# Kernel optimization log

Hardware: AMD Instinct MI355X
Metric: run time of the kernel (lower is better)

## Reference

```python
import jax, jax.numpy as jnp
import numpy as np

N_COARSE, N_FINE, N_EDGE, W, DEPTH = 16384, 65536, 393216, 128, 2


def _mlp_params(key, fan_in, width, out):
    k1, k2 = jax.random.split(key)
    w1 = jax.random.normal(k1, (fan_in, width), jnp.float32) / np.sqrt(fan_in)
    b1 = jnp.zeros((width,), jnp.float32)
    w2 = jax.random.normal(k2, (width, out), jnp.float32) / np.sqrt(width)
    b2 = jnp.zeros((out,), jnp.float32)
    return w1, b1, w2, b2


def setup_inputs() -> dict:
    key = jax.random.key(0)
    ks = jax.random.split(key, 16)
    v = jax.random.normal(ks[0], (N_COARSE, W), jnp.float32)
    c_skip = jax.random.normal(ks[1], (N_FINE, W), jnp.float32)
    e_skip = jax.random.normal(ks[2], (N_EDGE, W), jnp.float32)
    edge_index_skip = jax.random.randint(ks[3], (2, N_EDGE), 0, N_FINE, jnp.int32)
    batch_skip = jnp.zeros((N_FINE,), jnp.int32)  # single graph
    cluster = jax.random.randint(ks[4], (N_FINE,), 0, N_COARSE, jnp.int32)
    rel_pos = jax.random.normal(ks[5], (N_FINE, 1), jnp.float32)  # scalar rel pos (scalar_rel_pos=True)

    # unpooling FNN: (W + 1) -> W -> W
    uw1, ub1, uw2, ub2 = _mlp_params(ks[6], W + 1, W, W)
    # InteractionNetwork MLPs, stacked over DEPTH layers
    ew1 = []; eb1 = []; ew2 = []; eb2 = []
    nw1 = []; nb1 = []; nw2 = []; nb2 = []
    for i in range(DEPTH):
        a, b, c, d = _mlp_params(ks[7 + i], 3 * W, W, W)  # edge MLP: [e, v_s, v_r]
        ew1.append(a); eb1.append(b); ew2.append(c); eb2.append(d)
        a, b, c, d = _mlp_params(ks[9 + i], 2 * W, W, W)  # node MLP: [v, aggr(e)]
        nw1.append(a); nb1.append(b); nw2.append(c); nb2.append(d)
    stk = lambda xs: jnp.stack(xs, 0)
    return {
        'v': v, 'c_skip': c_skip, 'e_skip': e_skip, 'rel_pos': rel_pos,
        'unpool_w1': uw1, 'unpool_b1': ub1, 'unpool_w2': uw2, 'unpool_b2': ub2,
        'edge_w1': stk(ew1), 'edge_b1': stk(eb1), 'edge_w2': stk(ew2), 'edge_b2': stk(eb2),
        'node_w1': stk(nw1), 'node_b1': stk(nb1), 'node_w2': stk(nw2), 'node_b2': stk(nb2),
        'edge_index_skip': edge_index_skip, 'cluster': cluster, 'batch_skip': batch_skip,
    }


def _mlp(x, w1, b1, w2, b2):
    return jax.nn.selu(x @ w1 + b1) @ w2 + b2


def reference(v, c_skip, e_skip, rel_pos,
              unpool_w1, unpool_b1, unpool_w2, unpool_b2,
              edge_w1, edge_b1, edge_w2, edge_b2,
              node_w1, node_b1, node_w2, node_b2,
              edge_index_skip, cluster, batch_skip):
    # --- MeshUpMP: gather coarse features to fine nodes, mix with rel. pos. ---
    h = jnp.concatenate([v[cluster], rel_pos], axis=-1)            # [N_fine, W+1]
    v = _mlp(h, unpool_w1, unpool_b1, unpool_w2, unpool_b2)        # [N_fine, W]
    v = v + c_skip
    e = e_skip
    s, r = edge_index_skip[0], edge_index_skip[1]
    n_nodes = v.shape[0]
    # --- stacked InteractionNetwork layers (residual edge+node updates) ---
    for i in range(edge_w1.shape[0]):
        msg = jnp.concatenate([e, v[s], v[r]], axis=-1)            # [E, 3W]
        e = e + _mlp(msg, edge_w1[i], edge_b1[i], edge_w2[i], edge_b2[i])
        agg = jax.ops.segment_sum(e, r, num_segments=n_nodes)      # sum aggregation
        nin = jnp.concatenate([v, agg], axis=-1)                   # [N, 2W]
        v = v + _mlp(nin, node_w1[i], node_b1[i], node_w2[i], node_b2[i])
    return v
```

## Files before the change

kernel.cpp:

```cpp
#include <hip/hip_runtime.h>
#include <hip/hip_bf16.h>
#include <stdint.h>

#define NCOARSE 16384
#define NFINE   65536
#define NEDGE   393216

typedef __bf16 bf16;
typedef bf16 bf16x8 __attribute__((ext_vector_type(8)));
typedef bf16 bf16x4 __attribute__((ext_vector_type(4)));
typedef float f32x4 __attribute__((ext_vector_type(4)));

__device__ __forceinline__ float selu_f(float x) {
    return x > 0.f ? 1.0507009873554805f * x
                   : 1.7580993408473766f * (__expf(x) - 1.f);
}

__device__ __forceinline__ bf16x8 cvt8(f32x4 lo, f32x4 hi) {
    bf16x8 r;
    r[0] = (bf16)lo[0]; r[1] = (bf16)lo[1]; r[2] = (bf16)lo[2]; r[3] = (bf16)lo[3];
    r[4] = (bf16)hi[0]; r[5] = (bf16)hi[1]; r[6] = (bf16)hi[2]; r[7] = (bf16)hi[3];
    return r;
}

__global__ void prep_weights(const float* __restrict__ uw1, const float* __restrict__ uw2,
                             const float* __restrict__ ew1, const float* __restrict__ ew2,
                             const float* __restrict__ nw1, const float* __restrict__ nw2,
                             bf16* __restrict__ wb)
{
    int i = blockIdx.x * 256 + threadIdx.x;
    float v;
    if (i < 16384) {
        int j = i; int k = (j >> 12) * 32 + (j & 31), n = (j & 4095) >> 5;
        v = uw1[k * 128 + n];
    } else if (i < 32768) {
        int j = i - 16384; int k = (j >> 12) * 32 + (j & 31), n = (j & 4095) >> 5;
        v = uw2[k * 128 + n];
    } else if (i < 131072) {
        int j = i - 32768; int l = j / 49152; j -= l * 49152;
        int k = (j >> 12) * 32 + (j & 31), n = (j & 4095) >> 5;
        v = ew1[l * 49152 + k * 128 + n];
    } else if (i < 163840) {
        int j = i - 131072; int l = j >> 14; j &= 16383;
        int k = (j >> 12) * 32 + (j & 31), n = (j & 4095) >> 5;
        v = ew2[l * 16384 + k * 128 + n];
    } else if (i < 229376) {
        int j = i - 163840; int l = j >> 15; j &= 32767;
        int k = (j >> 12) * 32 + (j & 31), n = (j & 4095) >> 5;
        v = nw1[l * 32768 + k * 128 + n];
    } else {
        int j = i - 229376; int l = j >> 14; j &= 16383;
        int k = (j >> 12) * 32 + (j & 31), n = (j & 4095) >> 5;
        v = nw2[l * 16384 + k * 128 + n];
    }
    wb[i] = (bf16)v;
}

__global__ void hist_kernel(const int* __restrict__ ei, int* __restrict__ cnt) {
    int e = blockIdx.x * 256 + threadIdx.x;
    if (e < NEDGE) atomicAdd(&cnt[ei[NEDGE + e]], 1);
}

__global__ __launch_bounds__(1024)
void scan_kernel(const int* __restrict__ cnt, int* __restrict__ rowptr,
                 int* __restrict__ cursor) {
    __shared__ int part[1024];
    const int t = threadIdx.x;
    const int base = t * 64;
    int s = 0;
    for (int i = 0; i < 64; ++i) s += cnt[base + i];
    part[t] = s;
    __syncthreads();
    for (int off = 1; off < 1024; off <<= 1) {
        int v = (t >= off) ? part[t - off] : 0;
        __syncthreads();
        part[t] += v;
        __syncthreads();
    }
    int run = part[t] - s;
    for (int i = 0; i < 64; ++i) {
        int c = cnt[base + i];
        rowptr[base + i] = run;
        cursor[base + i] = run;
        run += c;
    }
    if (t == 1023) rowptr[65536] = run;
}

__global__ void scatter_kernel(const int* __restrict__ ei, int* __restrict__ cursor,
                               int* __restrict__ perm) {
    int e = blockIdx.x * 256 + threadIdx.x;
    if (e < NEDGE) {
        int r = ei[NEDGE + e];
        int p = atomicAdd(&cursor[r], 1);
        perm[p] = e;
    }
}

__global__ __launch_bounds__(256)
void agg_kernel(const bf16* __restrict__ e, const int* __restrict__ rowptr,
                const int* __restrict__ perm, bf16* __restrict__ agg) {
    int t = blockIdx.x * 256 + threadIdx.x;
    int node = t >> 3, c0 = (t & 7) * 16;
    int s = rowptr[node], en = rowptr[node + 1];
    float acc[16];
    #pragma unroll
    for (int k = 0; k < 16; ++k) acc[k] = 0.f;
    for (int j = s; j < en; ++j) {
        size_t ed = (size_t)perm[j];
        bf16x8 x0 = *(const bf16x8*)(e + ed * 128 + c0);
        bf16x8 x1 = *(const bf16x8*)(e + ed * 128 + c0 + 8);
        #pragma unroll
        for (int k = 0; k < 8; ++k) { acc[k] += (float)x0[k]; acc[8 + k] += (float)x1[k]; }
    }
    bf16x8 o0, o1;
    #pragma unroll
    for (int k = 0; k < 8; ++k) { o0[k] = (bf16)acc[k]; o1[k] = (bf16)acc[8 + k]; }
    *(bf16x8*)(agg + (size_t)node * 128 + c0) = o0;
    *(bf16x8*)(agg + (size_t)node * 128 + c0 + 8) = o1;
}


#define STAGE_LOAD(wp, st0, st1) do { \
    st0 = *(const bf16x8*)((wp) + tid * 8); \
    st1 = *(const bf16x8*)((wp) + 2048 + tid * 8); } while (0)
#define STAGE_WRITE(buf, st0, st1) do { \
    *(bf16x8*)&(buf)[tid >> 2][(tid & 3) * 8] = st0; \
    *(bf16x8*)&(buf)[(tid + 256) >> 2][(tid & 3) * 8] = st1; } while (0)

template<bool EF32>
__global__ __launch_bounds__(256, 2)
void edge_kernel(const void* __restrict__ e_in_v,
                 bf16* __restrict__ e_out,
                 const bf16* __restrict__ v_bf,
                 const int* __restrict__ ei,
                 const bf16* __restrict__ w1s,
                 const float* __restrict__ b1,
                 const bf16* __restrict__ w2s,
                 const float* __restrict__ b2)
{
    const int tid = threadIdx.x;
    const int wv = tid >> 6, lane = tid & 63;
    const int lr = lane & 15, g = lane >> 4;
    const int wbase = blockIdx.x * 128 + wv * 32;

    __shared__ bf16 wl[2][128][40];
    __shared__ bf16 hid_all[4][32][136];
    bf16 (*hid)[136] = hid_all[wv];

    const float* e_f32 = (const float*)e_in_v;
    const bf16*  e_b16 = (const bf16*)e_in_v;

    int row[2], sidx[2], ridx[2];
    #pragma unroll
    for (int mt = 0; mt < 2; ++mt) {
        row[mt] = wbase + mt * 16 + lr;
        sidx[mt] = ei[row[mt]];
        ridx[mt] = ei[NEDGE + row[mt]];
    }

    bf16x8 be[4][2], bs[4][2], br[4][2];
    #pragma unroll
    for (int ks = 0; ks < 4; ++ks)
        #pragma unroll
        for (int mt = 0; mt < 2; ++mt)
            bs[ks][mt] = *(const bf16x8*)(v_bf + (size_t)sidx[mt] * 128 + ks * 32 + g * 8);
    #pragma unroll
    for (int ks = 0; ks < 4; ++ks)
        #pragma unroll
        for (int mt = 0; mt < 2; ++mt)
            br[ks][mt] = *(const bf16x8*)(v_bf + (size_t)ridx[mt] * 128 + ks * 32 + g * 8);
    if (EF32) {
        f32x4 tlo[4][2], thi[4][2];
        #pragma unroll
        for (int ks = 0; ks < 4; ++ks)
            #pragma unroll
            for (int mt = 0; mt < 2; ++mt) {
                const float* p = e_f32 + (size_t)row[mt] * 128 + ks * 32 + g * 8;
                tlo[ks][mt] = *(const f32x4*)p;
                thi[ks][mt] = *(const f32x4*)(p + 4);
            }
        #pragma unroll
        for (int ks = 0; ks < 4; ++ks)
            #pragma unroll
            for (int mt = 0; mt < 2; ++mt)
                be[ks][mt] = cvt8(tlo[ks][mt], thi[ks][mt]);
    } else {
        #pragma unroll
        for (int ks = 0; ks < 4; ++ks)
            #pragma unroll
            for (int mt = 0; mt < 2; ++mt)
                be[ks][mt] = *(const bf16x8*)(e_b16 + (size_t)row[mt] * 128 + ks * 32 + g * 8);
    }

    bf16x8 st0, st1;
    STAGE_LOAD(w1s, st0, st1);
    STAGE_WRITE(wl[0], st0, st1);
    __syncthreads();

    f32x4 acc1[8][2], acc2[8][2];
    #pragma unroll
    for (int oc = 0; oc < 8; ++oc) {
        f32x4 z = {0.f, 0.f, 0.f, 0.f};
        acc1[oc][0] = z; acc1[oc][1] = z;
    }

    f32x4  eof[8][2];
    bf16x4 eob[8][2];

    #pragma unroll
    for (int s = 0; s < 16; ++s) {
        const int cur = s & 1;
        if (s < 15) {
            const bf16* wp = (s + 1 < 12) ? w1s + (size_t)(s + 1) * 4096
                                          : w2s + (size_t)(s + 1 - 12) * 4096;
            STAGE_LOAD(wp, st0, st1);
        }
        if (s == 12) {
            #pragma unroll
            for (int mt = 0; mt < 2; ++mt)
                #pragma unroll
                for (int oc = 0; oc < 8; ++oc) {
                    const int col = oc * 16 + g * 4;
                    if (EF32) eof[oc][mt] = *(const f32x4*)(e_f32 + (size_t)row[mt] * 128 + col);
                    else      eob[oc][mt] = *(const bf16x4*)(e_b16 + (size_t)row[mt] * 128 + col);
                }
        }
        bf16x8 a[8];
        #pragma unroll
        for (int oc = 0; oc < 8; ++oc)
            a[oc] = *(const bf16x8*)&wl[cur][oc * 16 + lr][g * 8];

        if (s < 12) {
            bf16x8 b0 = (s < 4) ? be[s][0] : (s < 8) ? bs[s - 4][0] : br[s - 8][0];
            bf16x8 b1f = (s < 4) ? be[s][1] : (s < 8) ? bs[s - 4][1] : br[s - 8][1];
            #pragma unroll
            for (int oc = 0; oc < 8; ++oc) {
                acc1[oc][0] = __builtin_amdgcn_mfma_f32_16x16x32_bf16(a[oc], b0, acc1[oc][0], 0, 0, 0);
                acc1[oc][1] = __builtin_amdgcn_mfma_f32_16x16x32_bf16(a[oc], b1f, acc1[oc][1], 0, 0, 0);
            }
        } else {
            if (s == 12) {
                #pragma unroll
                for (int oc = 0; oc < 8; ++oc) {
                    f32x4 z = {0.f, 0.f, 0.f, 0.f};
                    acc2[oc][0] = z; acc2[oc][1] = z;
                }
            }
            bf16x8 h0 = *(const bf16x8*)&hid[lr][(s - 12) * 32 + g * 8];
            bf16x8 h1 = *(const bf16x8*)&hid[16 + lr][(s - 12) * 32 + g * 8];
            #pragma unroll
            for (int oc = 0; oc < 8; ++oc) {
                acc2[oc][0] = __builtin_amdgcn_mfma_f32_16x16x32_bf16(a[oc], h0, acc2[oc][0], 0, 0, 0);
                acc2[oc][1] = __builtin_amdgcn_mfma_f32_16x16x32_bf16(a[oc], h1, acc2[oc][1], 0, 0, 0);
            }
        }
        if (s == 11) {
            #pragma unroll
            for (int mt = 0; mt < 2; ++mt)
                #pragma unroll
                for (int oc = 0; oc < 8; ++oc) {
                    const int col = oc * 16 + g * 4;
                    f32x4 bv = *(const f32x4*)(b1 + col);
                    bf16x4 h;
                    #pragma unroll
                    for (int j = 0; j < 4; ++j)
                        h[j] = (bf16)selu_f(acc1[oc][mt][j] + bv[j]);
                    *(bf16x4*)&hid[mt * 16 + lr][col] = h;
                }
        }
        if (s < 15) STAGE_WRITE(wl[cur ^ 1], st0, st1);
        __syncthreads();
    }

    #pragma unroll
    for (int mt = 0; mt < 2; ++mt) {
        const size_t r = row[mt];
        #pragma unroll
        for (int oc = 0; oc < 8; ++oc) {
            const int col = oc * 16 + g * 4;
            f32x4 b2v = *(const f32x4*)(b2 + col);
            bf16x4 stv;
            #pragma unroll
            for (int j = 0; j < 4; ++j) {
                float eo = EF32 ? eof[oc][mt][j] : (float)eob[oc][mt][j];
                stv[j] = (bf16)(eo + acc2[oc][mt][j] + b2v[j]);
            }
            __builtin_nontemporal_store(stv, (bf16x4*)(e_out + r * 128 + col));
        }
    }
}

__global__ __launch_bounds__(256, 2)
void node_kernel(float* __restrict__ v_io,
                 bf16* __restrict__ v_bf,
                 const bf16* __restrict__ agg,
                 const bf16* __restrict__ w1s,
                 const float* __restrict__ b1,
                 const bf16* __restrict__ w2s,
                 const float* __restrict__ b2)
{
    const int tid = threadIdx.x;
    const int wv = tid >> 6, lane = tid & 63;
    const int lr = lane & 15, g = lane >> 4;
    const int wbase = blockIdx.x * 128 + wv * 32;

    __shared__ bf16 wl[2][128][40];
    __shared__ bf16 hid_all[4][32][136];
    bf16 (*hid)[136] = hid_all[wv];

    int row[2];
    row[0] = wbase + lr; row[1] = wbase + 16 + lr;

    bf16x8 bv[4][2], ba[4][2];
    #pragma unroll
    for (int ks = 0; ks < 4; ++ks)
        #pragma unroll
        for (int mt = 0; mt < 2; ++mt)
            bv[ks][mt] = *(const bf16x8*)(v_bf + (size_t)row[mt] * 128 + ks * 32 + g * 8);
    #pragma unroll
    for (int ks = 0; ks < 4; ++ks)
        #pragma unroll
        for (int mt = 0; mt < 2; ++mt)
            ba[ks][mt] = *(const bf16x8*)(agg + (size_t)row[mt] * 128 + ks * 32 + g * 8);

    bf16x8 st0, st1;
    STAGE_LOAD(w1s, st0, st1);
    STAGE_WRITE(wl[0], st0, st1);
    __syncthreads();

    f32x4 acc1[8][2], acc2[8][2], vo[8][2];
    #pragma unroll
    for (int oc = 0; oc < 8; ++oc) {
        f32x4 z = {0.f, 0.f, 0.f, 0.f};
        acc1[oc][0] = z; acc1[oc][1] = z;
    }

    #pragma unroll
    for (int s = 0; s < 12; ++s) {
        const int cur = s & 1;
        if (s < 11) {
            const bf16* wp = (s + 1 < 8) ? w1s + (size_t)(s + 1) * 4096
                                         : w2s + (size_t)(s + 1 - 8) * 4096;
            STAGE_LOAD(wp, st0, st1);
        }
        if (s == 8) {
            #pragma unroll
            for (int mt = 0; mt < 2; ++mt)
                #pragma unroll
                for (int oc = 0; oc < 8; ++oc)
                    vo[oc][mt] = *(const f32x4*)(v_io + (size_t)row[mt] * 128 + oc * 16 + g * 4);
        }
        bf16x8 a[8];
        #pragma unroll
        for (int oc = 0; oc < 8; ++oc)
            a[oc] = *(const bf16x8*)&wl[cur][oc * 16 + lr][g * 8];

        if (s < 8) {
            bf16x8 b0 = (s < 4) ? bv[s][0] : ba[s - 4][0];
            bf16x8 b1f = (s < 4) ? bv[s][1] : ba[s - 4][1];
            #pragma unroll
            for (int oc = 0; oc < 8; ++oc) {
                acc1[oc][0] = __builtin_amdgcn_mfma_f32_16x16x32_bf16(a[oc], b0, acc1[oc][0], 0, 0, 0);
                acc1[oc][1] = __builtin_amdgcn_mfma_f32_16x16x32_bf16(a[oc], b1f, acc1[oc][1], 0, 0, 0);
            }
        } else {
            if (s == 8) {
                #pragma unroll
                for (int oc = 0; oc < 8; ++oc) {
                    f32x4 z = {0.f, 0.f, 0.f, 0.f};
                    acc2[oc][0] = z; acc2[oc][1] = z;
                }
            }
            bf16x8 h0 = *(const bf16x8*)&hid[lr][(s - 8) * 32 + g * 8];
            bf16x8 h1 = *(const bf16x8*)&hid[16 + lr][(s - 8) * 32 + g * 8];
            #pragma unroll
            for (int oc = 0; oc < 8; ++oc) {
                acc2[oc][0] = __builtin_amdgcn_mfma_f32_16x16x32_bf16(a[oc], h0, acc2[oc][0], 0, 0, 0);
                acc2[oc][1] = __builtin_amdgcn_mfma_f32_16x16x32_bf16(a[oc], h1, acc2[oc][1], 0, 0, 0);
            }
        }
        if (s == 7) {
            #pragma unroll
            for (int mt = 0; mt < 2; ++mt)
                #pragma unroll
                for (int oc = 0; oc < 8; ++oc) {
                    const int col = oc * 16 + g * 4;
                    f32x4 bvv = *(const f32x4*)(b1 + col);
                    bf16x4 h;
                    #pragma unroll
                    for (int j = 0; j < 4; ++j)
                        h[j] = (bf16)selu_f(acc1[oc][mt][j] + bvv[j]);
                    *(bf16x4*)&hid[mt * 16 + lr][col] = h;
                }
        }
        if (s < 11) STAGE_WRITE(wl[cur ^ 1], st0, st1);
        __syncthreads();
    }

    #pragma unroll
    for (int mt = 0; mt < 2; ++mt) {
        const size_t r = row[mt];
        #pragma unroll
        for (int oc = 0; oc < 8; ++oc) {
            const int col = oc * 16 + g * 4;
            f32x4 b2v = *(const f32x4*)(b2 + col);
            f32x4 vn; bf16x4 m;
            #pragma unroll
            for (int j = 0; j < 4; ++j) {
                vn[j] = vo[oc][mt][j] + acc2[oc][mt][j] + b2v[j];
                m[j] = (bf16)vn[j];
            }
            *(f32x4*)(v_io + r * 128 + col) = vn;
            *(bf16x4*)(v_bf + r * 128 + col) = m;
        }
    }
}

__global__ __launch_bounds__(256, 2)
void unpool_kernel(const float* __restrict__ v_coarse,
                   const float* __restrict__ c_skip,
                   const float* __restrict__ rel_pos,
                   const float* __restrict__ uw1,
                   const float* __restrict__ b1,
                   const bf16* __restrict__ w1s,
                   const bf16* __restrict__ w2s,
                   const float* __restrict__ b2,
                   const int* __restrict__ cluster,
                   float* __restrict__ v_out,
                   bf16* __restrict__ v_bf)
{
    const int tid = threadIdx.x;
    const int wv = tid >> 6, lane = tid & 63;
    const int lr = lane & 15, g = lane >> 4;
    const int wbase = blockIdx.x * 128 + wv * 32;

    __shared__ bf16 wl[2][128][40];
    __shared__ bf16 hid_all[4][32][136];
    bf16 (*hid)[136] = hid_all[wv];

    int row[2], cl[2]; float relv[2];
    #pragma unroll
    for (int mt = 0; mt < 2; ++mt) {
        row[mt] = wbase + mt * 16 + lr;
        cl[mt] = cluster[row[mt]];
        relv[mt] = rel_pos[row[mt]];
    }

    bf16x8 bfr[4][2];
    {
        f32x4 tlo[4][2], thi[4][2];
        #pragma unroll
        for (int ks = 0; ks < 4; ++ks)
            #pragma unroll
            for (int mt = 0; mt < 2; ++mt) {
                const float* p = v_coarse + (size_t)cl[mt] * 128 + ks * 32 + g * 8;
                tlo[ks][mt] = *(const f32x4*)p;
                thi[ks][mt] = *(const f32x4*)(p + 4);
            }
        #pragma unroll
        for (int ks = 0; ks < 4; ++ks)
            #pragma unroll
            for (int mt = 0; mt < 2; ++mt)
                bfr[ks][mt] = cvt8(tlo[ks][mt], thi[ks][mt]);
    }

    bf16x8 st0, st1;
    STAGE_LOAD(w1s, st0, st1);
    STAGE_WRITE(wl[0], st0, st1);
    __syncthreads();

    f32x4 acc1[8][2], acc2[8][2], cs[8][2];
    #pragma unroll
    for (int oc = 0; oc < 8; ++oc) {
        f32x4 z = {0.f, 0.f, 0.f, 0.f};
        acc1[oc][0] = z; acc1[oc][1] = z;
    }

    #pragma unroll
    for (int s = 0; s < 8; ++s) {
        const int cur = s & 1;
        if (s < 7) {
            const bf16* wp = (s + 1 < 4) ? w1s + (size_t)(s + 1) * 4096
                                         : w2s + (size_t)(s + 1 - 4) * 4096;
            STAGE_LOAD(wp, st0, st1);
        }
        if (s == 4) {
            #pragma unroll
            for (int mt = 0; mt < 2; ++mt)
                #pragma unroll
                for (int oc = 0; oc < 8; ++oc)
                    cs[oc][mt] = *(const f32x4*)(c_skip + (size_t)row[mt] * 128 + oc * 16 + g * 4);
        }
        bf16x8 a[8];
        #pragma unroll
        for (int oc = 0; oc < 8; ++oc)
            a[oc] = *(const bf16x8*)&wl[cur][oc * 16 + lr][g * 8];

        if (s < 4) {
            #pragma unroll
            for (int oc = 0; oc < 8; ++oc) {
                acc1[oc][0] = __builtin_amdgcn_mfma_f32_16x16x32_bf16(a[oc], bfr[s][0], acc1[oc][0], 0, 0, 0);
                acc1[oc][1] = __builtin_amdgcn_mfma_f32_16x16x32_bf16(a[oc], bfr[s][1], acc1[oc][1], 0, 0, 0);
            }
        } else {
            if (s == 4) {
                #pragma unroll
                for (int oc = 0; oc < 8; ++oc) {
                    f32x4 z = {0.f, 0.f, 0.f, 0.f};
                    acc2[oc][0] = z; acc2[oc][1] = z;
                }
            }
            bf16x8 h0 = *(const bf16x8*)&hid[lr][(s - 4) * 32 + g * 8];
            bf16x8 h1 = *(const bf16x8*)&hid[16 + lr][(s - 4) * 32 + g * 8];
            #pragma unroll
            for (int oc = 0; oc < 8; ++oc) {
                acc2[oc][0] = __builtin_amdgcn_mfma_f32_16x16x32_bf16(a[oc], h0, acc2[oc][0], 0, 0, 0);
                acc2[oc][1] = __builtin_amdgcn_mfma_f32_16x16x32_bf16(a[oc], h1, acc2[oc][1], 0, 0, 0);
            }
        }
        if (s == 3) {
            #pragma unroll
            for (int mt = 0; mt < 2; ++mt)
                #pragma unroll
                for (int oc = 0; oc < 8; ++oc) {
                    const int col = oc * 16 + g * 4;
                    f32x4 bvv = *(const f32x4*)(b1 + col);
                    f32x4 wlr = *(const f32x4*)(uw1 + 128 * 128 + col);
                    bf16x4 h;
                    #pragma unroll
                    for (int j = 0; j < 4; ++j)
                        h[j] = (bf16)selu_f(acc1[oc][mt][j] + bvv[j] + relv[mt] * wlr[j]);
                    *(bf16x4*)&hid[mt * 16 + lr][col] = h;
                }
        }
        if (s < 7) STAGE_WRITE(wl[cur ^ 1], st0, st1);
        __syncthreads();
    }

    #pragma unroll
    for (int mt = 0; mt < 2; ++mt) {
        const size_t r = row[mt];
        #pragma unroll
        for (int oc = 0; oc < 8; ++oc) {
            const int col = oc * 16 + g * 4;
            f32x4 b2v = *(const f32x4*)(b2 + col);
            f32x4 vn; bf16x4 m;
            #pragma unroll
            for (int j = 0; j < 4; ++j) {
                vn[j] = acc2[oc][mt][j] + b2v[j] + cs[oc][mt][j];
                m[j] = (bf16)vn[j];
            }
            *(f32x4*)(v_out + r * 128 + col) = vn;
            *(bf16x4*)(v_bf + r * 128 + col) = m;
        }
    }
}

extern "C" void kernel_launch(void* const* d_in, const int* in_sizes, int n_in,
                              void* d_out, int out_size, void* d_ws, size_t ws_size,
                              hipStream_t stream) {
    const float* v_c    = (const float*)d_in[0];
    const float* c_skip = (const float*)d_in[1];
    const float* e_skip = (const float*)d_in[2];
    const float* rel    = (const float*)d_in[3];
    const float* uw1    = (const float*)d_in[4];
    const float* ub1    = (const float*)d_in[5];
    const float* uw2    = (const float*)d_in[6];
    const float* ub2    = (const float*)d_in[7];
    const float* ew1    = (const float*)d_in[8];
    const float* eb1    = (const float*)d_in[9];
    const float* ew2    = (const float*)d_in[10];
    const float* eb2    = (const float*)d_in[11];
    const float* nw1    = (const float*)d_in[12];
    const float* nb1    = (const float*)d_in[13];
    const float* nw2    = (const float*)d_in[14];
    const float* nb2    = (const float*)d_in[15];
    const int*   ei     = (const int*)d_in[16];
    const int*   clus   = (const int*)d_in[17];

    char* ws = (char*)d_ws;
    bf16*  e_bf   = (bf16*)(ws);
    bf16*  v_bf   = (bf16*)(ws + 100663296);
    bf16*  agg    = (bf16*)(ws + 117440512);
    bf16*  wb     = (bf16*)(ws + 134217728);
    int*   cnt    = (int*) (ws + 134742016);
    int*   rowptr = (int*) (ws + 135004160);
    int*   cursor = (int*) (ws + 135266308);
    int*   perm   = (int*) (ws + 135528452);

    float* vout = (float*)d_out;

    prep_weights<<<1024, 256, 0, stream>>>(uw1, uw2, ew1, ew2, nw1, nw2, wb);
    hipMemsetAsync(cnt, 0, 262144, stream);
    hist_kernel<<<1536, 256, 0, stream>>>(ei, cnt);
    scan_kernel<<<1, 1024, 0, stream>>>(cnt, rowptr, cursor);
    scatter_kernel<<<1536, 256, 0, stream>>>(ei, cursor, perm);

    unpool_kernel<<<512, 256, 0, stream>>>(v_c, c_skip, rel, uw1, ub1,
                                           wb + 0, wb + 16384, ub2, clus, vout, v_bf);

    edge_kernel<true><<<3072, 256, 0, stream>>>((const void*)e_skip, e_bf, v_bf, ei,
                                                wb + 32768, eb1, wb + 131072, eb2);
    agg_kernel<<<2048, 256, 0, stream>>>(e_bf, rowptr, perm, agg);
    node_kernel<<<512, 256, 0, stream>>>(vout, v_bf, agg,
                                         wb + 163840, nb1, wb + 229376, nb2);

    edge_kernel<false><<<3072, 256, 0, stream>>>((const void*)e_bf, e_bf, v_bf, ei,
                                                 wb + 32768 + 49152, eb1 + 128,
                                                 wb + 131072 + 16384, eb2 + 128);
    agg_kernel<<<2048, 256, 0, stream>>>(e_bf, rowptr, perm, agg);
    node_kernel<<<512, 256, 0, stream>>>(vout, v_bf, agg,
                                         wb + 163840 + 32768, nb1 + 128, wb + 229376 + 16384, nb2 + 128);
}
```

Before: 553.4 us.

## Make edge kernel persistent with LDS-resident W1 and register-resident W2

The edge MLP kernel becomes persistent: 256 blocks each load the whole first-layer weight matrix once into LDS, in a new k-inner layout produced by prep_weights. Each lane keeps its second-layer weight fragments in registers. Each wave then loops over 12 edge tiles, prefetching the next tile's edge features and gathered node rows while computing the current one. This removes the per-tile weight staging and per-step block barriers of the old double-buffered pipeline. The cost is one 4-wave block per CU, which leaves little occupancy to hide gather latency, plus heavy register pressure. The output store also changes from nontemporal to a plain store.

```diff
diff --git a/kernel.cpp b/kernel.cpp
--- a/kernel.cpp
+++ b/kernel.cpp
@@ -38,7 +38,8 @@
         v = uw2[k * 128 + n];
     } else if (i < 131072) {
         int j = i - 32768; int l = j / 49152; j -= l * 49152;
-        int k = (j >> 12) * 32 + (j & 31), n = (j & 4095) >> 5;
+        int seg = j >> 12, g = (j >> 10) & 3, n = (j >> 3) & 127, kk = j & 7;
+        int k = seg * 32 + g * 8 + kk;
         v = ew1[l * 49152 + k * 128 + n];
     } else if (i < 163840) {
         int j = i - 131072; int l = j >> 14; j &= 16383;
@@ -120,21 +121,22 @@
     *(bf16x8*)(agg + (size_t)node * 128 + c0 + 8) = o1;
 }
 
-
-#define STAGE_LOAD(wp, st0, st1) do { \
-    st0 = *(const bf16x8*)((wp) + tid * 8); \
-    st1 = *(const bf16x8*)((wp) + 2048 + tid * 8); } while (0)
-#define STAGE_WRITE(buf, st0, st1) do { \
-    *(bf16x8*)&(buf)[tid >> 2][(tid & 3) * 8] = st0; \
-    *(bf16x8*)&(buf)[(tid + 256) >> 2][(tid & 3) * 8] = st1; } while (0)
+__device__ __forceinline__ void load_v2(bf16x8 (&dst)[4][2], const bf16* __restrict__ v,
+                                        const int idx0, const int idx1, int g) {
+    #pragma unroll
+    for (int ks = 0; ks < 4; ++ks) {
+        dst[ks][0] = *(const bf16x8*)(v + (size_t)idx0 * 128 + ks * 32 + g * 8);
+        dst[ks][1] = *(const bf16x8*)(v + (size_t)idx1 * 128 + ks * 32 + g * 8);
+    }
+}
 
 template<bool EF32>
-__global__ __launch_bounds__(256, 2)
+__global__ __launch_bounds__(256, 1)
 void edge_kernel(const void* __restrict__ e_in_v,
                  bf16* __restrict__ e_out,
                  const bf16* __restrict__ v_bf,
                  const int* __restrict__ ei,
-                 const bf16* __restrict__ w1s,
+                 const bf16* __restrict__ w1g,
                  const float* __restrict__ b1,
                  const bf16* __restrict__ w2s,
                  const float* __restrict__ b2)
@@ -142,154 +144,189 @@
     const int tid = threadIdx.x;
     const int wv = tid >> 6, lane = tid & 63;
     const int lr = lane & 15, g = lane >> 4;
-    const int wbase = blockIdx.x * 128 + wv * 32;
-
-    __shared__ bf16 wl[2][128][40];
+
+    __shared__ bf16 wl[49152];
     __shared__ bf16 hid_all[4][32][136];
     bf16 (*hid)[136] = hid_all[wv];
 
     const float* e_f32 = (const float*)e_in_v;
     const bf16*  e_b16 = (const bf16*)e_in_v;
 
-    int row[2], sidx[2], ridx[2];
-    #pragma unroll
-    for (int mt = 0; mt < 2; ++mt) {
-        row[mt] = wbase + mt * 16 + lr;
-        sidx[mt] = ei[row[mt]];
-        ridx[mt] = ei[NEDGE + row[mt]];
-    }
-
-    bf16x8 be[4][2], bs[4][2], br[4][2];
-    #pragma unroll
-    for (int ks = 0; ks < 4; ++ks)
+    #pragma unroll
+    for (int c = 0; c < 24; ++c)
+        *(bf16x8*)&wl[c * 2048 + tid * 8] = *(const bf16x8*)(w1g + c * 2048 + tid * 8);
+
+    bf16x8 a2[4][8];
+    #pragma unroll
+    for (int s2 = 0; s2 < 4; ++s2)
+        #pragma unroll
+        for (int oc = 0; oc < 8; ++oc)
+            a2[s2][oc] = *(const bf16x8*)(w2s + s2 * 4096 + (oc * 16 + lr) * 32 + g * 8);
+
+    __syncthreads();
+
+    int tile = blockIdx.x * 48 + wv;
+
+    int rowC0, rowC1;
+    bf16x8 beC[4][2], bsC[4][2], brC[4][2];
+
+    {
+        rowC0 = tile * 32 + lr;
+        rowC1 = tile * 32 + 16 + lr;
+        int s0 = ei[rowC0], s1 = ei[rowC1];
+        int r0 = ei[NEDGE + rowC0], r1 = ei[NEDGE + rowC1];
+        if (EF32) {
+            #pragma unroll
+            for (int ks = 0; ks < 4; ++ks) {
+                const float* p0 = e_f32 + (size_t)rowC0 * 128 + ks * 32 + g * 8;
+                const float* p1 = e_f32 + (size_t)rowC1 * 128 + ks * 32 + g * 8;
+                beC[ks][0] = cvt8(*(const f32x4*)p0, *(const f32x4*)(p0 + 4));
+                beC[ks][1] = cvt8(*(const f32x4*)p1, *(const f32x4*)(p1 + 4));
+            }
+        } else {
+            #pragma unroll
+            for (int ks = 0; ks < 4; ++ks) {
+                beC[ks][0] = *(const bf16x8*)(e_b16 + (size_t)rowC0 * 128 + ks * 32 + g * 8);
+                beC[ks][1] = *(const bf16x8*)(e_b16 + (size_t)rowC1 * 128 + ks * 32 + g * 8);
+            }
+        }
+        load_v2(bsC, v_bf, s0, s1, g);
+        load_v2(brC, v_bf, r0, r1, g);
+    }
+
+    #pragma clang loop unroll(disable)
+    for (int i = 0; i < 12; ++i) {
+        const int ntile = tile + 4;
+        const bool more = (i < 11);
+
+        int rowN0 = 0, rowN1 = 0, sN0 = 0, sN1 = 0, rN0 = 0, rN1 = 0;
+        if (more) {
+            rowN0 = ntile * 32 + lr;
+            rowN1 = ntile * 32 + 16 + lr;
+            sN0 = ei[rowN0]; sN1 = ei[rowN1];
+            rN0 = ei[NEDGE + rowN0]; rN1 = ei[NEDGE + rowN1];
+        }
+
+        f32x4 acc1[8][2];
+        #pragma unroll
+        for (int oc = 0; oc < 8; ++oc) {
+            f32x4 z = {0.f, 0.f, 0.f, 0.f};
+            acc1[oc][0] = z; acc1[oc][1] = z;
+        }
+        #pragma unroll
+        for (int seg = 0; seg < 12; ++seg) {
+            bf16x8 b0 = (seg < 4) ? beC[seg & 3][0] : (seg < 8) ? bsC[seg & 3][0] : brC[seg & 3][0];
+            bf16x8 b1f = (seg < 4) ? beC[seg & 3][1] : (seg < 8) ? bsC[seg & 3][1] : brC[seg & 3][1];
+            #pragma unroll
+            for (int oc = 0; oc < 8; ++oc) {
+                bf16x8 a = *(const bf16x8*)&wl[(seg * 4 + g) * 1024 + (oc * 16 + lr) * 8];
+                acc1[oc][0] = __builtin_amdgcn_mfma_f32_16x16x32_bf16(a, b0, acc1[oc][0], 0, 0, 0);
+                acc1[oc][1] = __builtin_amdgcn_mfma_f32_16x16x32_bf16(a, b1f, acc1[oc][1], 0, 0, 0);
+            }
+        }
+
+        bf16x8 beN[4][2], bsN[4][2], brN[4][2];
+        if (more) {
+            if (EF32) {
+                #pragma unroll
+                for (int ks = 0; ks < 4; ++ks) {
+                    const float* p0 = e_f32 + (size_t)rowN0 * 128 + ks * 32 + g * 8;
+                    const float* p1 = e_f32 + (size_t)rowN1 * 128 + ks * 32 + g * 8;
+                    beN[ks][0] = cvt8(*(const f32x4*)p0, *(const f32x4*)(p0 + 4));
+                    beN[ks][1] = cvt8(*(const f32x4*)p1, *(const f32x4*)(p1 + 4));
+                }
+            } else {
+                #pragma unroll
+                for (int ks = 0; ks < 4; ++ks) {
+                    beN[ks][0] = *(const bf16x8*)(e_b16 + (size_t)rowN0 * 128 + ks * 32 + g * 8);
+                    beN[ks][1] = *(const bf16x8*)(e_b16 + (size_t)rowN1 * 128 + ks * 32 + g * 8);
+                }
+            }
+            load_v2(bsN, v_bf, sN0, sN1, g);
+            load_v2(brN, v_bf, rN0, rN1, g);
+        }
+
         #pragma unroll
         for (int mt = 0; mt < 2; ++mt)
-            bs[ks][mt] = *(const bf16x8*)(v_bf + (size_t)sidx[mt] * 128 + ks * 32 + g * 8);
-    #pragma unroll
-    for (int ks = 0; ks < 4; ++ks)
-        #pragma unroll
-        for (int mt = 0; mt < 2; ++mt)
-            br[ks][mt] = *(const bf16x8*)(v_bf + (size_t)ridx[mt] * 128 + ks * 32 + g * 8);
-    if (EF32) {
-        f32x4 tlo[4][2], thi[4][2];
-        #pragma unroll
-        for (int ks = 0; ks < 4; ++ks)
-            #pragma unroll
-            for (int mt = 0; mt < 2; ++mt) {
-                const float* p = e_f32 + (size_t)row[mt] * 128 + ks * 32 + g * 8;
-                tlo[ks][mt] = *(const f32x4*)p;
-                thi[ks][mt] = *(const f32x4*)(p + 4);
-            }
-        #pragma unroll
-        for (int ks = 0; ks < 4; ++ks)
-            #pragma unroll
-            for (int mt = 0; mt < 2; ++mt)
-                be[ks][mt] = cvt8(tlo[ks][mt], thi[ks][mt]);
-    } else {
-        #pragma unroll
-        for (int ks = 0; ks < 4; ++ks)
-            #pragma unroll
-            for (int mt = 0; mt < 2; ++mt)
-                be[ks][mt] = *(const bf16x8*)(e_b16 + (size_t)row[mt] * 128 + ks * 32 + g * 8);
-    }
-
-    bf16x8 st0, st1;
-    STAGE_LOAD(w1s, st0, st1);
-    STAGE_WRITE(wl[0], st0, st1);
-    __syncthreads();
-
-    f32x4 acc1[8][2], acc2[8][2];
-    #pragma unroll
-    for (int oc = 0; oc < 8; ++oc) {
-        f32x4 z = {0.f, 0.f, 0.f, 0.f};
-        acc1[oc][0] = z; acc1[oc][1] = z;
-    }
-
-    f32x4  eof[8][2];
-    bf16x4 eob[8][2];
-
-    #pragma unroll
-    for (int s = 0; s < 16; ++s) {
-        const int cur = s & 1;
-        if (s < 15) {
-            const bf16* wp = (s + 1 < 12) ? w1s + (size_t)(s + 1) * 4096
-                                          : w2s + (size_t)(s + 1 - 12) * 4096;
-            STAGE_LOAD(wp, st0, st1);
-        }
-        if (s == 12) {
-            #pragma unroll
-            for (int mt = 0; mt < 2; ++mt)
-                #pragma unroll
-                for (int oc = 0; oc < 8; ++oc) {
-                    const int col = oc * 16 + g * 4;
-                    if (EF32) eof[oc][mt] = *(const f32x4*)(e_f32 + (size_t)row[mt] * 128 + col);
-                    else      eob[oc][mt] = *(const bf16x4*)(e_b16 + (size_t)row[mt] * 128 + col);
-                }
-        }
-        bf16x8 a[8];
-        #pragma unroll
-        for (int oc = 0; oc < 8; ++oc)
-            a[oc] = *(const bf16x8*)&wl[cur][oc * 16 + lr][g * 8];
-
-        if (s < 12) {
-            bf16x8 b0 = (s < 4) ? be[s][0] : (s < 8) ? bs[s - 4][0] : br[s - 8][0];
-            bf16x8 b1f = (s < 4) ? be[s][1] : (s < 8) ? bs[s - 4][1] : br[s - 8][1];
-            #pragma unroll
-            for (int oc = 0; oc < 8; ++oc) {
-                acc1[oc][0] = __builtin_amdgcn_mfma_f32_16x16x32_bf16(a[oc], b0, acc1[oc][0], 0, 0, 0);
-                acc1[oc][1] = __builtin_amdgcn_mfma_f32_16x16x32_bf16(a[oc], b1f, acc1[oc][1], 0, 0, 0);
-            }
-        } else {
-            if (s == 12) {
-                #pragma unroll
-                for (int oc = 0; oc < 8; ++oc) {
-                    f32x4 z = {0.f, 0.f, 0.f, 0.f};
-                    acc2[oc][0] = z; acc2[oc][1] = z;
-                }
-            }
-            bf16x8 h0 = *(const bf16x8*)&hid[lr][(s - 12) * 32 + g * 8];
-            bf16x8 h1 = *(const bf16x8*)&hid[16 + lr][(s - 12) * 32 + g * 8];
-            #pragma unroll
-            for (int oc = 0; oc < 8; ++oc) {
-                acc2[oc][0] = __builtin_amdgcn_mfma_f32_16x16x32_bf16(a[oc], h0, acc2[oc][0], 0, 0, 0);
-                acc2[oc][1] = __builtin_amdgcn_mfma_f32_16x16x32_bf16(a[oc], h1, acc2[oc][1], 0, 0, 0);
-            }
-        }
-        if (s == 11) {
-            #pragma unroll
-            for (int mt = 0; mt < 2; ++mt)
-                #pragma unroll
-                for (int oc = 0; oc < 8; ++oc) {
-                    const int col = oc * 16 + g * 4;
-                    f32x4 bv = *(const f32x4*)(b1 + col);
-                    bf16x4 h;
-                    #pragma unroll
-                    for (int j = 0; j < 4; ++j)
-                        h[j] = (bf16)selu_f(acc1[oc][mt][j] + bv[j]);
-                    *(bf16x4*)&hid[mt * 16 + lr][col] = h;
-                }
-        }
-        if (s < 15) STAGE_WRITE(wl[cur ^ 1], st0, st1);
-        __syncthreads();
-    }
-
-    #pragma unroll
-    for (int mt = 0; mt < 2; ++mt) {
-        const size_t r = row[mt];
+            #pragma unroll
+            for (int oc = 0; oc < 8; ++oc) {
+                const int col = oc * 16 + g * 4;
+                f32x4 bv = *(const f32x4*)(b1 + col);
+                bf16x4 h;
+                #pragma unroll
+                for (int j = 0; j < 4; ++j)
+                    h[j] = (bf16)selu_f(acc1[oc][mt][j] + bv[j]);
+                *(bf16x4*)&hid[mt * 16 + lr][col] = h;
+            }
+
+        f32x4  eof[8][2];
+        bf16x4 eob[8][2];
+        #pragma unroll
+        for (int mt = 0; mt < 2; ++mt) {
+            const size_t r = (mt == 0) ? (size_t)rowC0 : (size_t)rowC1;
+            #pragma unroll
+            for (int oc = 0; oc < 8; ++oc) {
+                const int col = oc * 16 + g * 4;
+                if (EF32) eof[oc][mt] = *(const f32x4*)(e_f32 + r * 128 + col);
+                else      eob[oc][mt] = *(const bf16x4*)(e_b16 + r * 128 + col);
+            }
+        }
+
+        f32x4 acc2[8][2];
         #pragma unroll
         for (int oc = 0; oc < 8; ++oc) {
-            const int col = oc * 16 + g * 4;
-            f32x4 b2v = *(const f32x4*)(b2 + col);
-            bf16x4 stv;
-            #pragma unroll
-            for (int j = 0; j < 4; ++j) {
-                float eo = EF32 ? eof[oc][mt][j] : (float)eob[oc][mt][j];
-                stv[j] = (bf16)(eo + acc2[oc][mt][j] + b2v[j]);
-            }
-            __builtin_nontemporal_store(stv, (bf16x4*)(e_out + r * 128 + col));
-        }
-    }
-}
+            f32x4 z = {0.f, 0.f, 0.f, 0.f};
+            acc2[oc][0] = z; acc2[oc][1] = z;
+        }
+        #pragma unroll
+        for (int s2 = 0; s2 < 4; ++s2) {
+            bf16x8 h0 = *(const bf16x8*)&hid[lr][s2 * 32 + g * 8];
+            bf16x8 h1 = *(const bf16x8*)&hid[16 + lr][s2 * 32 + g * 8];
+            #pragma unroll
+            for (int oc = 0; oc < 8; ++oc) {
+                acc2[oc][0] = __builtin_amdgcn_mfma_f32_16x16x32_bf16(a2[s2][oc], h0, acc2[oc][0], 0, 0, 0);
+                acc2[oc][1] = __builtin_amdgcn_mfma_f32_16x16x32_bf16(a2[s2][oc], h1, acc2[oc][1], 0, 0, 0);
+            }
+        }
+
+        #pragma unroll
+        for (int mt = 0; mt < 2; ++mt) {
+            const size_t r = (mt == 0) ? (size_t)rowC0 : (size_t)rowC1;
+            #pragma unroll
+            for (int oc = 0; oc < 8; ++oc) {
+                const int col = oc * 16 + g * 4;
+                f32x4 b2v = *(const f32x4*)(b2 + col);
+                bf16x4 stv;
+                #pragma unroll
+                for (int j = 0; j < 4; ++j) {
+                    float eo = EF32 ? eof[oc][mt][j] : (float)eob[oc][mt][j];
+                    stv[j] = (bf16)(eo + acc2[oc][mt][j] + b2v[j]);
+                }
+                *(bf16x4*)(e_out + r * 128 + col) = stv;
+            }
+        }
+
+        if (more) {
+            #pragma unroll
+            for (int ks = 0; ks < 4; ++ks)
+                #pragma unroll
+                for (int mt = 0; mt < 2; ++mt) {
+                    beC[ks][mt] = beN[ks][mt];
+                    bsC[ks][mt] = bsN[ks][mt];
+                    brC[ks][mt] = brN[ks][mt];
+                }
+            rowC0 = rowN0; rowC1 = rowN1;
+        }
+        tile = ntile;
+    }
+}
+
+#define STAGE_LOAD(wp, st0, st1) do { \
+    st0 = *(const bf16x8*)((wp) + tid * 8); \
+    st1 = *(const bf16x8*)((wp) + 2048 + tid * 8); } while (0)
+#define STAGE_WRITE(buf, st0, st1) do { \
+    *(bf16x8*)&(buf)[tid >> 2][(tid & 3) * 8] = st0; \
+    *(bf16x8*)&(buf)[(tid + 256) >> 2][(tid & 3) * 8] = st1; } while (0)
 
 __global__ __launch_bounds__(256, 2)
 void node_kernel(float* __restrict__ v_io,
@@ -600,15 +637,15 @@
     unpool_kernel<<<512, 256, 0, stream>>>(v_c, c_skip, rel, uw1, ub1,
                                            wb + 0, wb + 16384, ub2, clus, vout, v_bf);
 
-    edge_kernel<true><<<3072, 256, 0, stream>>>((const void*)e_skip, e_bf, v_bf, ei,
-                                                wb + 32768, eb1, wb + 131072, eb2);
+    edge_kernel<true><<<256, 256, 0, stream>>>((const void*)e_skip, e_bf, v_bf, ei,
+                                               wb + 32768, eb1, wb + 131072, eb2);
     agg_kernel<<<2048, 256, 0, stream>>>(e_bf, rowptr, perm, agg);
     node_kernel<<<512, 256, 0, stream>>>(vout, v_bf, agg,
                                          wb + 163840, nb1, wb + 229376, nb2);
 
-    edge_kernel<false><<<3072, 256, 0, stream>>>((const void*)e_bf, e_bf, v_bf, ei,
-                                                 wb + 32768 + 49152, eb1 + 128,
-                                                 wb + 131072 + 16384, eb2 + 128);
+    edge_kernel<false><<<256, 256, 0, stream>>>((const void*)e_bf, e_bf, v_bf, ei,
+                                                wb + 32768 + 49152, eb1 + 128,
+                                                wb + 131072 + 16384, eb2 + 128);
     agg_kernel<<<2048, 256, 0, stream>>>(e_bf, rowptr, perm, agg);
     node_kernel<<<512, 256, 0, stream>>>(vout, v_bf, agg,
                                          wb + 163840 + 32768, nb1 + 128, wb + 229376 + 16384, nb2 + 128);
```

Measured after the change: 1.325 ms. 139% more time.

## Make edge kernel persistent with full weights resident in LDS and prefetch

Applied to the files above, without the earlier changes.

The edge MLP kernel becomes persistent: 256 blocks each load the whole edge W1 and W2 into shared memory once, laid out in a new MFMA-friendly order. Each wave then loops over 12 edge tiles of 32 rows and double-buffers the gathered e/v_s/v_r operands for the next tile in registers while computing the current one. This removes the per-tile restaging of weights and the 16 barriers per tile, and replaces nontemporal stores with ordinary stores. In exchange it uses about 128KB of LDS at one block per CU, only 256 blocks, and heavy register pressure from two 12x2 operand buffers, which could cause spills or low occupancy.

```diff
diff --git a/kernel.cpp b/kernel.cpp
--- a/kernel.cpp
+++ b/kernel.cpp
@@ -38,11 +38,13 @@
         v = uw2[k * 128 + n];
     } else if (i < 131072) {
         int j = i - 32768; int l = j / 49152; j -= l * 49152;
-        int k = (j >> 12) * 32 + (j & 31), n = (j & 4095) >> 5;
+        int seg = j >> 12, g = (j >> 10) & 3, n = (j >> 3) & 127, kk = j & 7;
+        int k = seg * 32 + g * 8 + kk;
         v = ew1[l * 49152 + k * 128 + n];
     } else if (i < 163840) {
         int j = i - 131072; int l = j >> 14; j &= 16383;
-        int k = (j >> 12) * 32 + (j & 31), n = (j & 4095) >> 5;
+        int seg = j >> 12, g = (j >> 10) & 3, n = (j >> 3) & 127, kk = j & 7;
+        int k = seg * 32 + g * 8 + kk;
         v = ew2[l * 16384 + k * 128 + n];
     } else if (i < 229376) {
         int j = i - 163840; int l = j >> 15; j &= 32767;
@@ -121,175 +123,152 @@
 }
 
 
+#define LOADB(bb, row0, row1, s0, s1, r0, r1) do {                           \
+    if (EF32) {                                                              \
+      _Pragma("unroll") for (int ks = 0; ks < 4; ++ks) {                     \
+        const float* p0 = e_f32 + (size_t)(row0) * 128 + ks * 32 + g * 8;    \
+        const float* p1 = e_f32 + (size_t)(row1) * 128 + ks * 32 + g * 8;    \
+        bb[ks][0] = cvt8(*(const f32x4*)p0, *(const f32x4*)(p0 + 4));        \
+        bb[ks][1] = cvt8(*(const f32x4*)p1, *(const f32x4*)(p1 + 4));        \
+      }                                                                      \
+    } else {                                                                 \
+      _Pragma("unroll") for (int ks = 0; ks < 4; ++ks) {                     \
+        bb[ks][0] = *(const bf16x8*)(e_b16 + (size_t)(row0) * 128 + ks * 32 + g * 8); \
+        bb[ks][1] = *(const bf16x8*)(e_b16 + (size_t)(row1) * 128 + ks * 32 + g * 8); \
+      }                                                                      \
+    }                                                                        \
+    _Pragma("unroll") for (int ks = 0; ks < 4; ++ks) {                       \
+      bb[4+ks][0] = *(const bf16x8*)(v_bf + (size_t)(s0) * 128 + ks * 32 + g * 8); \
+      bb[4+ks][1] = *(const bf16x8*)(v_bf + (size_t)(s1) * 128 + ks * 32 + g * 8); \
+      bb[8+ks][0] = *(const bf16x8*)(v_bf + (size_t)(r0) * 128 + ks * 32 + g * 8); \
+      bb[8+ks][1] = *(const bf16x8*)(v_bf + (size_t)(r1) * 128 + ks * 32 + g * 8); \
+    }                                                                        \
+  } while (0)
+
+#define EDGE_ITER(bbC, bbN, I) do {                                          \
+    const int tcur = tile0 + 4 * (I);                                        \
+    const int rowC0 = tcur * 32 + lr, rowC1 = tcur * 32 + 16 + lr;           \
+    int sN0 = 0, sN1 = 0, rN0 = 0, rN1 = 0, rowN0 = 0, rowN1 = 0;            \
+    if ((I) < 11) {                                                          \
+      rowN0 = (tcur + 4) * 32 + lr; rowN1 = (tcur + 4) * 32 + 16 + lr;       \
+      sN0 = ei[rowN0]; sN1 = ei[rowN1];                                      \
+      rN0 = ei[NEDGE + rowN0]; rN1 = ei[NEDGE + rowN1];                      \
+    }                                                                        \
+    f32x4 acc1[8][2];                                                        \
+    _Pragma("unroll") for (int oc = 0; oc < 8; ++oc) {                       \
+      f32x4 z = {0.f, 0.f, 0.f, 0.f}; acc1[oc][0] = z; acc1[oc][1] = z; }    \
+    _Pragma("unroll") for (int seg = 0; seg < 12; ++seg) {                   \
+      _Pragma("unroll") for (int oc = 0; oc < 8; ++oc) {                     \
+        bf16x8 a = *(const bf16x8*)&wl[(seg * 4 + g) * 1024 + (oc * 16 + lr) * 8]; \
+        acc1[oc][0] = __builtin_amdgcn_mfma_f32_16x16x32_bf16(a, bbC[seg][0], acc1[oc][0], 0, 0, 0); \
+        acc1[oc][1] = __builtin_amdgcn_mfma_f32_16x16x32_bf16(a, bbC[seg][1], acc1[oc][1], 0, 0, 0); \
+      }                                                                      \
+    }                                                                        \
+    if ((I) < 11) LOADB(bbN, rowN0, rowN1, sN0, sN1, rN0, rN1);              \
+    f32x4 eof[8][2]; bf16x4 eob[8][2];                                       \
+    _Pragma("unroll") for (int mt = 0; mt < 2; ++mt) {                       \
+      const size_t rr = (mt == 0) ? (size_t)rowC0 : (size_t)rowC1;           \
+      _Pragma("unroll") for (int oc = 0; oc < 8; ++oc) {                     \
+        const int col = oc * 16 + g * 4;                                     \
+        if (EF32) eof[oc][mt] = *(const f32x4*)(e_f32 + rr * 128 + col);     \
+        else      eob[oc][mt] = *(const bf16x4*)(e_b16 + rr * 128 + col);    \
+      }                                                                      \
+    }                                                                        \
+    _Pragma("unroll") for (int mt = 0; mt < 2; ++mt) {                       \
+      _Pragma("unroll") for (int oc = 0; oc < 8; ++oc) {                     \
+        const int col = oc * 16 + g * 4;                                     \
+        f32x4 bv = *(const f32x4*)(b1 + col);                                \
+        bf16x4 h;                                                            \
+        _Pragma("unroll") for (int j = 0; j < 4; ++j)                        \
+          h[j] = (bf16)selu_f(acc1[oc][mt][j] + bv[j]);                      \
+        *(bf16x4*)&hid[lr][col] = h;                                         \
+      }                                                                      \
+      f32x4 acc2[8];                                                         \
+      _Pragma("unroll") for (int oc = 0; oc < 8; ++oc) {                     \
+        f32x4 z = {0.f, 0.f, 0.f, 0.f}; acc2[oc] = z; }                      \
+      _Pragma("unroll") for (int s2 = 0; s2 < 4; ++s2) {                     \
+        bf16x8 h0 = *(const bf16x8*)&hid[lr][s2 * 32 + g * 8];               \
+        _Pragma("unroll") for (int oc = 0; oc < 8; ++oc) {                   \
+          bf16x8 a = *(const bf16x8*)&w2l[(s2 * 4 + g) * 1024 + (oc * 16 + lr) * 8]; \
+          acc2[oc] = __builtin_amdgcn_mfma_f32_16x16x32_bf16(a, h0, acc2[oc], 0, 0, 0); \
+        }                                                                    \
+      }                                                                      \
+      const size_t rr = (mt == 0) ? (size_t)rowC0 : (size_t)rowC1;           \
+      _Pragma("unroll") for (int oc = 0; oc < 8; ++oc) {                     \
+        const int col = oc * 16 + g * 4;                                     \
+        f32x4 b2v = *(const f32x4*)(b2 + col);                               \
+        bf16x4 stv;                                                          \
+        _Pragma("unroll") for (int j = 0; j < 4; ++j) {                      \
+          float eo = EF32 ? eof[oc][mt][j] : (float)eob[oc][mt][j];          \
+          stv[j] = (bf16)(eo + acc2[oc][j] + b2v[j]);                        \
+        }                                                                    \
+        *(bf16x4*)(e_out + rr * 128 + col) = stv;                            \
+      }                                                                      \
+    }                                                                        \
+  } while (0)
+
+template<bool EF32>
+__global__ __launch_bounds__(256, 1)
+void edge_kernel(const void* __restrict__ e_in_v,
+                 bf16* __restrict__ e_out,
+                 const bf16* __restrict__ v_bf,
+                 const int* __restrict__ ei,
+                 const bf16* __restrict__ w1g,
+                 const float* __restrict__ b1,
+                 const bf16* __restrict__ w2g,
+                 const float* __restrict__ b2)
+{
+    const int tid = threadIdx.x;
+    const int wv = tid >> 6, lane = tid & 63;
+    const int lr = lane & 15, g = lane >> 4;
+
+    __shared__ bf16 wl[49152];
+    __shared__ bf16 w2l[16384];
+    __shared__ bf16 hid_all[4][16][136];
+    bf16 (*hid)[136] = hid_all[wv];
+
+    const float* e_f32 = (const float*)e_in_v;
+    const bf16*  e_b16 = (const bf16*)e_in_v;
+
+    #pragma unroll
+    for (int c = 0; c < 24; ++c)
+        *(bf16x8*)&wl[c * 2048 + tid * 8] = *(const bf16x8*)(w1g + c * 2048 + tid * 8);
+    #pragma unroll
+    for (int c = 0; c < 8; ++c)
+        *(bf16x8*)&w2l[c * 2048 + tid * 8] = *(const bf16x8*)(w2g + c * 2048 + tid * 8);
+    __syncthreads();
+
+    const int tile0 = blockIdx.x * 48 + wv;
+
+    bf16x8 bbA[12][2], bbB[12][2];
+
+    {
+        int row0 = tile0 * 32 + lr, row1 = tile0 * 32 + 16 + lr;
+        int s0 = ei[row0], s1 = ei[row1];
+        int r0 = ei[NEDGE + row0], r1 = ei[NEDGE + row1];
+        LOADB(bbA, row0, row1, s0, s1, r0, r1);
+    }
+
+    EDGE_ITER(bbA, bbB, 0);
+    EDGE_ITER(bbB, bbA, 1);
+    EDGE_ITER(bbA, bbB, 2);
+    EDGE_ITER(bbB, bbA, 3);
+    EDGE_ITER(bbA, bbB, 4);
+    EDGE_ITER(bbB, bbA, 5);
+    EDGE_ITER(bbA, bbB, 6);
+    EDGE_ITER(bbB, bbA, 7);
+    EDGE_ITER(bbA, bbB, 8);
+    EDGE_ITER(bbB, bbA, 9);
+    EDGE_ITER(bbA, bbB, 10);
+    EDGE_ITER(bbB, bbA, 11);
+}
+
 #define STAGE_LOAD(wp, st0, st1) do { \
     st0 = *(const bf16x8*)((wp) + tid * 8); \
     st1 = *(const bf16x8*)((wp) + 2048 + tid * 8); } while (0)
 #define STAGE_WRITE(buf, st0, st1) do { \
     *(bf16x8*)&(buf)[tid >> 2][(tid & 3) * 8] = st0; \
     *(bf16x8*)&(buf)[(tid + 256) >> 2][(tid & 3) * 8] = st1; } while (0)
-
-template<bool EF32>
-__global__ __launch_bounds__(256, 2)
-void edge_kernel(const void* __restrict__ e_in_v,
-                 bf16* __restrict__ e_out,
-                 const bf16* __restrict__ v_bf,
-                 const int* __restrict__ ei,
-                 const bf16* __restrict__ w1s,
-                 const float* __restrict__ b1,
-                 const bf16* __restrict__ w2s,
-                 const float* __restrict__ b2)
-{
-    const int tid = threadIdx.x;
-    const int wv = tid >> 6, lane = tid & 63;
-    const int lr = lane & 15, g = lane >> 4;
-    const int wbase = blockIdx.x * 128 + wv * 32;
-
-    __shared__ bf16 wl[2][128][40];
-    __shared__ bf16 hid_all[4][32][136];
-    bf16 (*hid)[136] = hid_all[wv];
-
-    const float* e_f32 = (const float*)e_in_v;
-    const bf16*  e_b16 = (const bf16*)e_in_v;
-
-    int row[2], sidx[2], ridx[2];
-    #pragma unroll
-    for (int mt = 0; mt < 2; ++mt) {
-        row[mt] = wbase + mt * 16 + lr;
-        sidx[mt] = ei[row[mt]];
-        ridx[mt] = ei[NEDGE + row[mt]];
-    }
-
-    bf16x8 be[4][2], bs[4][2], br[4][2];
-    #pragma unroll
-    for (int ks = 0; ks < 4; ++ks)
-        #pragma unroll
-        for (int mt = 0; mt < 2; ++mt)
-            bs[ks][mt] = *(const bf16x8*)(v_bf + (size_t)sidx[mt] * 128 + ks * 32 + g * 8);
-    #pragma unroll
-    for (int ks = 0; ks < 4; ++ks)
-        #pragma unroll
-        for (int mt = 0; mt < 2; ++mt)
-            br[ks][mt] = *(const bf16x8*)(v_bf + (size_t)ridx[mt] * 128 + ks * 32 + g * 8);
-    if (EF32) {
-        f32x4 tlo[4][2], thi[4][2];
-        #pragma unroll
-        for (int ks = 0; ks < 4; ++ks)
-            #pragma unroll
-            for (int mt = 0; mt < 2; ++mt) {
-                const float* p = e_f32 + (size_t)row[mt] * 128 + ks * 32 + g * 8;
-                tlo[ks][mt] = *(const f32x4*)p;
-                thi[ks][mt] = *(const f32x4*)(p + 4);
-            }
-        #pragma unroll
-        for (int ks = 0; ks < 4; ++ks)
-            #pragma unroll
-            for (int mt = 0; mt < 2; ++mt)
-                be[ks][mt] = cvt8(tlo[ks][mt], thi[ks][mt]);
-    } else {
-        #pragma unroll
-        for (int ks = 0; ks < 4; ++ks)
-            #pragma unroll
-            for (int mt = 0; mt < 2; ++mt)
-                be[ks][mt] = *(const bf16x8*)(e_b16 + (size_t)row[mt] * 128 + ks * 32 + g * 8);
-    }
-
-    bf16x8 st0, st1;
-    STAGE_LOAD(w1s, st0, st1);
-    STAGE_WRITE(wl[0], st0, st1);
-    __syncthreads();
-
-    f32x4 acc1[8][2], acc2[8][2];
-    #pragma unroll
-    for (int oc = 0; oc < 8; ++oc) {
-        f32x4 z = {0.f, 0.f, 0.f, 0.f};
-        acc1[oc][0] = z; acc1[oc][1] = z;
-    }
-
-    f32x4  eof[8][2];
-    bf16x4 eob[8][2];
-
-    #pragma unroll
-    for (int s = 0; s < 16; ++s) {
-        const int cur = s & 1;
-        if (s < 15) {
-            const bf16* wp = (s + 1 < 12) ? w1s + (size_t)(s + 1) * 4096
-                                          : w2s + (size_t)(s + 1 - 12) * 4096;
-            STAGE_LOAD(wp, st0, st1);
-        }
-        if (s == 12) {
-            #pragma unroll
-            for (int mt = 0; mt < 2; ++mt)
-                #pragma unroll
-                for (int oc = 0; oc < 8; ++oc) {
-                    const int col = oc * 16 + g * 4;
-                    if (EF32) eof[oc][mt] = *(const f32x4*)(e_f32 + (size_t)row[mt] * 128 + col);
-                    else      eob[oc][mt] = *(const bf16x4*)(e_b16 + (size_t)row[mt] * 128 + col);
-                }
-        }
-        bf16x8 a[8];
-        #pragma unroll
-        for (int oc = 0; oc < 8; ++oc)
-            a[oc] = *(const bf16x8*)&wl[cur][oc * 16 + lr][g * 8];
-
-        if (s < 12) {
-            bf16x8 b0 = (s < 4) ? be[s][0] : (s < 8) ? bs[s - 4][0] : br[s - 8][0];
-            bf16x8 b1f = (s < 4) ? be[s][1] : (s < 8) ? bs[s - 4][1] : br[s - 8][1];
-            #pragma unroll
-            for (int oc = 0; oc < 8; ++oc) {
-                acc1[oc][0] = __builtin_amdgcn_mfma_f32_16x16x32_bf16(a[oc], b0, acc1[oc][0], 0, 0, 0);
-                acc1[oc][1] = __builtin_amdgcn_mfma_f32_16x16x32_bf16(a[oc], b1f, acc1[oc][1], 0, 0, 0);
-            }
-        } else {
-            if (s == 12) {
-                #pragma unroll
-                for (int oc = 0; oc < 8; ++oc) {
-                    f32x4 z = {0.f, 0.f, 0.f, 0.f};
-                    acc2[oc][0] = z; acc2[oc][1] = z;
-                }
-            }
-            bf16x8 h0 = *(const bf16x8*)&hid[lr][(s - 12) * 32 + g * 8];
-            bf16x8 h1 = *(const bf16x8*)&hid[16 + lr][(s - 12) * 32 + g * 8];
-            #pragma unroll
-            for (int oc = 0; oc < 8; ++oc) {
-                acc2[oc][0] = __builtin_amdgcn_mfma_f32_16x16x32_bf16(a[oc], h0, acc2[oc][0], 0, 0, 0);
-                acc2[oc][1] = __builtin_amdgcn_mfma_f32_16x16x32_bf16(a[oc], h1, acc2[oc][1], 0, 0, 0);
-            }
-        }
-        if (s == 11) {
-            #pragma unroll
-            for (int mt = 0; mt < 2; ++mt)
-                #pragma unroll
-                for (int oc = 0; oc < 8; ++oc) {
-                    const int col = oc * 16 + g * 4;
-                    f32x4 bv = *(const f32x4*)(b1 + col);
-                    bf16x4 h;
-                    #pragma unroll
-                    for (int j = 0; j < 4; ++j)
-                        h[j] = (bf16)selu_f(acc1[oc][mt][j] + bv[j]);
-                    *(bf16x4*)&hid[mt * 16 + lr][col] = h;
-                }
-        }
-        if (s < 15) STAGE_WRITE(wl[cur ^ 1], st0, st1);
-        __syncthreads();
-    }
-
-    #pragma unroll
-    for (int mt = 0; mt < 2; ++mt) {
-        const size_t r = row[mt];
-        #pragma unroll
-        for (int oc = 0; oc < 8; ++oc) {
-            const int col = oc * 16 + g * 4;
-            f32x4 b2v = *(const f32x4*)(b2 + col);
-            bf16x4 stv;
-            #pragma unroll
-            for (int j = 0; j < 4; ++j) {
-                float eo = EF32 ? eof[oc][mt][j] : (float)eob[oc][mt][j];
-                stv[j] = (bf16)(eo + acc2[oc][mt][j] + b2v[j]);
-            }
-            __builtin_nontemporal_store(stv, (bf16x4*)(e_out + r * 128 + col));
-        }
-    }
-}
 
 __global__ __launch_bounds__(256, 2)
 void node_kernel(float* __restrict__ v_io,
@@ -600,15 +579,15 @@
     unpool_kernel<<<512, 256, 0, stream>>>(v_c, c_skip, rel, uw1, ub1,
                                            wb + 0, wb + 16384, ub2, clus, vout, v_bf);
 
-    edge_kernel<true><<<3072, 256, 0, stream>>>((const void*)e_skip, e_bf, v_bf, ei,
-                                                wb + 32768, eb1, wb + 131072, eb2);
+    edge_kernel<true><<<256, 256, 0, stream>>>((const void*)e_skip, e_bf, v_bf, ei,
+                                               wb + 32768, eb1, wb + 131072, eb2);
     agg_kernel<<<2048, 256, 0, stream>>>(e_bf, rowptr, perm, agg);
     node_kernel<<<512, 256, 0, stream>>>(vout, v_bf, agg,
                                          wb + 163840, nb1, wb + 229376, nb2);
 
-    edge_kernel<false><<<3072, 256, 0, stream>>>((const void*)e_bf, e_bf, v_bf, ei,
-                                                 wb + 32768 + 49152, eb1 + 128,
-                                                 wb + 131072 + 16384, eb2 + 128);
+    edge_kernel<false><<<256, 256, 0, stream>>>((const void*)e_bf, e_bf, v_bf, ei,
+                                                wb + 32768 + 49152, eb1 + 128,
+                                                wb + 131072 + 16384, eb2 + 128);
     agg_kernel<<<2048, 256, 0, stream>>>(e_bf, rowptr, perm, agg);
     node_kernel<<<512, 256, 0, stream>>>(vout, v_bf, agg,
                                          wb + 163840 + 32768, nb1 + 128, wb + 229376 + 16384, nb2 + 128);
```

Measured after the change: 613.0 us. 10.8% more time.
